# Performance work log

Measured on AMD Instinct MI355X. Metric: run time of the kernel, lower is better.

## Reference

```python
import jax, jax.numpy as jnp
import numpy as np

EPS = 1e-7
LAMBDA_RANK = 0.5
NEG = -1e30  # finite stand-in for -inf (keeps logsumexp grads finite)

B = 8192
N_BINS = 4


def setup_inputs() -> dict:
    key = jax.random.key(0)
    k1, k2, k3, k4 = jax.random.split(key, 4)
    outputs = jax.random.normal(k1, (B, N_BINS), dtype=jnp.float32)
    t = jax.random.uniform(k2, (B,), dtype=jnp.float32) * 100.0  # survival times
    y = jax.random.randint(k3, (B,), 0, N_BINS, dtype=jnp.int32)  # interval index
    c = jax.random.randint(k4, (B,), 0, 2, dtype=jnp.int32)       # 0=event, 1=censored
    return {"outputs": outputs, "t": t, "y": y, "c": c}


def reference(outputs, t, y, c):
    dt = outputs.dtype
    # ---- NLL survival loss ----
    hazards = jax.nn.sigmoid(outputs)                       # [B, K]
    S = jnp.cumprod(1.0 - hazards, axis=1)                  # [B, K]
    S_pad = jnp.concatenate([jnp.ones((outputs.shape[0], 1), dt), S], axis=1)  # [B, K+1]
    yv = y[:, None].astype(jnp.int32)
    s_prev = jnp.clip(jnp.take_along_axis(S_pad, yv, axis=1), EPS)
    h_this = jnp.clip(jnp.take_along_axis(hazards, yv, axis=1), EPS)
    s_this = jnp.clip(jnp.take_along_axis(S_pad, yv + 1, axis=1), EPS)
    cf = c[:, None].astype(dt)
    uncensored = -(1.0 - cf) * (jnp.log(s_prev) + jnp.log(h_this))
    censored = -cf * jnp.log(s_this)
    loss_nll = (censored + uncensored).mean()  # alpha == 0, reduction == 'mean'

    # ---- pairwise rank loss (vectorized over all i) ----
    risk = -jnp.sum(S, axis=1)                               # [B]
    event = (c == 0)                                         # [B] bool
    pair_mask = t[None, :] > t[:, None]                      # [B, B]; (i, j): t_j > t_i
    masked = jnp.where(pair_mask, risk[None, :], NEG)        # [B, B]
    lse = jax.nn.logsumexp(masked, axis=1)                   # [B]
    valid = event & jnp.any(pair_mask, axis=1)               # rows contributing
    contrib = jnp.where(valid, lse - risk, jnp.zeros((), dt))
    count = jnp.sum(valid.astype(dt))
    loss_rank = jnp.where(count > 0, contrib.sum() / jnp.maximum(count, 1.0), jnp.zeros((), dt))

    return loss_nll + LAMBDA_RANK * loss_rank
```

## Files before the change

kernel.cpp:

```cpp
#include <hip/hip_runtime.h>

#define BROWS 8192
#define EPSF 1e-7f
#define NBLK 256
#define RPB 32
#define TPB 1024

__device__ __forceinline__ float wave_reduce_sum(float v) {
    #pragma unroll
    for (int off = 32; off > 0; off >>= 1) v += __shfl_xor(v, off, 64);
    return v;
}
__device__ __forceinline__ float rcp_fast(float x) { return __builtin_amdgcn_rcpf(x); }

__device__ __forceinline__ float aload(const float* p) {
    return __hip_atomic_load(p, __ATOMIC_RELAXED, __HIP_MEMORY_SCOPE_AGENT);
}
__device__ __forceinline__ void astore(float* p, float v) {
    __hip_atomic_store(p, v, __ATOMIC_RELAXED, __HIP_MEMORY_SCOPE_AGENT);
}

__global__ __launch_bounds__(TPB, 4) void fused_kernel(
        const float4* __restrict__ outputs, const float* __restrict__ t,
        const int* __restrict__ y, const int* __restrict__ c,
        float* __restrict__ part, float* __restrict__ out) {
    __shared__ float2 te[BROWS];
    int tid = threadIdx.x, lane = tid & 63, wave = tid >> 6;
    int b = blockIdx.x;
    int rowbase = b * RPB;

    #pragma unroll
    for (int u = 0; u < BROWS / TPB; ++u) {
        int j = tid + u * TPB;
        float4 o = outputs[j];
        float q0 = rcp_fast(1.f + __expf(o.x));
        float q1 = rcp_fast(1.f + __expf(o.y));
        float q2 = rcp_fast(1.f + __expf(o.z));
        float q3 = rcp_fast(1.f + __expf(o.w));
        float S1 = q0, S2 = S1 * q1, S3 = S2 * q2, S4 = S3 * q3;
        float risk = -(S1 + S2 + S3 + S4);
        te[j] = make_float2(t[j], __expf(risk));
    }
    __syncthreads();

    float t0 = te[rowbase + 2 * wave].x;
    float t1 = te[rowbase + 2 * wave + 1].x;
    float a0 = 0.f, a1 = 0.f;
    const float4* te4 = (const float4*)te;
    #pragma unroll 8
    for (int k = lane; k < BROWS / 2; k += 64) {
        float4 q = te4[k];
        a0 += (q.x > t0) ? q.y : 0.f;
        a1 += (q.x > t1) ? q.y : 0.f;
        a0 += (q.z > t0) ? q.w : 0.f;
        a1 += (q.z > t1) ? q.w : 0.f;
    }
    a0 = wave_reduce_sum(a0);
    a1 = wave_reduce_sum(a1);
    __syncthreads();

    float* wsum = (float*)te;
    if (lane == 0) { wsum[2 * wave] = a0; wsum[2 * wave + 1] = a1; }
    __syncthreads();

    if (wave == 0) {
        float contrib = 0.f, cnt = 0.f, nll = 0.f;
        if (lane < RPB) {
            int row = rowbase + lane;
            float s = wsum[lane];
            float4 o = outputs[row];
            float q0 = rcp_fast(1.f + __expf(o.x));
            float q1 = rcp_fast(1.f + __expf(o.y));
            float q2 = rcp_fast(1.f + __expf(o.z));
            float q3 = rcp_fast(1.f + __expf(o.w));
            float S1 = q0, S2 = S1 * q1, S3 = S2 * q2, S4 = S3 * q3;
            float risk = -(S1 + S2 + S3 + S4);
            int yi = y[row], ci = c[row];
            float s_prev = (yi == 0) ? 1.f : (yi == 1) ? S1 : (yi == 2) ? S2 : S3;
            float s_this = (yi == 0) ? S1  : (yi == 1) ? S2 : (yi == 2) ? S3 : S4;
            float xsel   = (yi == 0) ? o.x : (yi == 1) ? o.y : (yi == 2) ? o.z : o.w;
            float h_this = rcp_fast(1.f + __expf(-xsel));
            float cf = (float)ci;
            nll = -cf * __logf(fmaxf(s_this, EPSF))
                  - (1.f - cf) * (__logf(fmaxf(s_prev, EPSF)) + __logf(fmaxf(h_this, EPSF)));
            bool valid = (ci == 0) && (s > 0.f);
            contrib = valid ? (__logf(s) - risk) : 0.f;
            cnt     = valid ? 1.f : 0.f;
        }
        contrib = wave_reduce_sum(contrib);
        cnt     = wave_reduce_sum(cnt);
        nll     = wave_reduce_sum(nll);
        if (lane == 0) {
            astore(&part[b * 4 + 0], contrib);
            astore(&part[b * 4 + 1], cnt);
            astore(&part[b * 4 + 2], nll);
            asm volatile("s_waitcnt vmcnt(0)" ::: "memory");
            astore(&part[b * 4 + 3], 1.0f);
        }
    }

    if (b == 0 && wave == 0) {
        int p0 = lane * 4;
        for (int sweep = 0; sweep < (1 << 17); ++sweep) {
            int ok = 1;
            #pragma unroll
            for (int k = 0; k < 4; ++k)
                ok &= (aload(&part[(p0 + k) * 4 + 3]) == 1.0f);
            if (__all(ok)) break;
            __builtin_amdgcn_s_sleep(8);
        }
        asm volatile("" ::: "memory");
        float rs = 0.f, cs = 0.f, ns = 0.f;
        #pragma unroll
        for (int k = 0; k < 4; ++k) {
            int pb = (p0 + k) * 4;
            rs += aload(&part[pb + 0]);
            cs += aload(&part[pb + 1]);
            ns += aload(&part[pb + 2]);
        }
        rs = wave_reduce_sum(rs);
        cs = wave_reduce_sum(cs);
        ns = wave_reduce_sum(ns);
        if (lane == 0) {
            float loss_nll  = ns / (float)BROWS;
            float loss_rank = (cs > 0.f) ? (rs / fmaxf(cs, 1.f)) : 0.f;
            out[0] = loss_nll + 0.5f * loss_rank;
        }
    }
}

extern "C" void kernel_launch(void* const* d_in, const int* in_sizes, int n_in,
                              void* d_out, int out_size, void* d_ws, size_t ws_size,
                              hipStream_t stream) {
    const float4* outputs = (const float4*)d_in[0];
    const float*  t       = (const float*)d_in[1];
    const int*    y       = (const int*)d_in[2];
    const int*    c       = (const int*)d_in[3];
    float* out  = (float*)d_out;
    float* part = (float*)d_ws;

    fused_kernel<<<NBLK, TPB, 0, stream>>>(outputs, t, y, c, part, out);
}
```

Measured before the change: 16.56 us.

## Replace O(B^2) pairwise sums with bucketed suffix-sum plus in-bucket correction

Each block now bins every exp(risk) into 4096 time buckets with shared-memory atomics and builds a suffix sum with a wave scan. Each row reads the suffix beyond its bucket and adds same-bucket entries through a staged list, replacing the full 8192-element scan per row. Block count halves to 128 with 64 rows each. The bucket scale 40.96 assumes t lies in [0,100), which matches the test inputs. Values outside that range are clamped into the edge buckets, still corrected by the in-bucket list, and rows are lost only if the stage capacity of 2048 overflows.

New measurement: 42.20 us. 155% more time.

```diff
diff --git a/kernel.cpp b/kernel.cpp
--- a/kernel.cpp
+++ b/kernel.cpp
@@ -1,36 +1,60 @@
 #include <hip/hip_runtime.h>
 
 #define BROWS 8192
-#define EPSF 1e-7f
-#define NBLK 256
-#define RPB 32
-#define TPB 1024
+#define NB    4096
+#define EPSF  1e-7f
+#define NBLK  128
+#define RPB   64
+#define TPB   1024
+#define IPT   (BROWS / TPB)
+#define SCAP  2048
 
 __device__ __forceinline__ float wave_reduce_sum(float v) {
     #pragma unroll
     for (int off = 32; off > 0; off >>= 1) v += __shfl_xor(v, off, 64);
     return v;
 }
+__device__ __forceinline__ float wave_incl_scan(float v, int lane) {
+    #pragma unroll
+    for (int off = 1; off < 64; off <<= 1) {
+        float u = __shfl_up(v, off, 64);
+        if (lane >= off) v += u;
+    }
+    return v;
+}
 __device__ __forceinline__ float rcp_fast(float x) { return __builtin_amdgcn_rcpf(x); }
-
 __device__ __forceinline__ float aload(const float* p) {
     return __hip_atomic_load(p, __ATOMIC_RELAXED, __HIP_MEMORY_SCOPE_AGENT);
 }
 __device__ __forceinline__ void astore(float* p, float v) {
     __hip_atomic_store(p, v, __ATOMIC_RELAXED, __HIP_MEMORY_SCOPE_AGENT);
 }
+__device__ __forceinline__ int bucket_of(float t) {
+    int b = (int)(t * 40.96f);
+    return min(max(b, 0), NB - 1);
+}
 
 __global__ __launch_bounds__(TPB, 4) void fused_kernel(
         const float4* __restrict__ outputs, const float* __restrict__ t,
         const int* __restrict__ y, const int* __restrict__ c,
         float* __restrict__ part, float* __restrict__ out) {
-    __shared__ float2 te[BROWS];
+    __shared__ float esum[NB];
+    __shared__ float suf[NB + 1];
+    __shared__ unsigned char rowhit[NB];
+    __shared__ float2 stage_te[SCAP];
+    __shared__ unsigned short stage_b[SCAP];
+    __shared__ int stage_n;
+    __shared__ float wtot[16];
+
     int tid = threadIdx.x, lane = tid & 63, wave = tid >> 6;
-    int b = blockIdx.x;
-    int rowbase = b * RPB;
+    int rowbase = blockIdx.x * RPB;
 
+    for (int k = tid; k < NB; k += TPB) { esum[k] = 0.f; rowhit[k] = 0; }
+    if (tid == 0) stage_n = 0;
+
+    float it_t[IPT], it_e[IPT]; int it_b[IPT];
     #pragma unroll
-    for (int u = 0; u < BROWS / TPB; ++u) {
+    for (int u = 0; u < IPT; ++u) {
         int j = tid + u * TPB;
         float4 o = outputs[j];
         float q0 = rcp_fast(1.f + __expf(o.x));
@@ -39,80 +63,102 @@
         float q3 = rcp_fast(1.f + __expf(o.w));
         float S1 = q0, S2 = S1 * q1, S3 = S2 * q2, S4 = S3 * q3;
         float risk = -(S1 + S2 + S3 + S4);
-        te[j] = make_float2(t[j], __expf(risk));
+        float tj = t[j];
+        it_t[u] = tj;
+        it_e[u] = __expf(risk);
+        it_b[u] = bucket_of(tj);
     }
     __syncthreads();
 
-    float t0 = te[rowbase + 2 * wave].x;
-    float t1 = te[rowbase + 2 * wave + 1].x;
-    float a0 = 0.f, a1 = 0.f;
-    const float4* te4 = (const float4*)te;
-    #pragma unroll 8
-    for (int k = lane; k < BROWS / 2; k += 64) {
-        float4 q = te4[k];
-        a0 += (q.x > t0) ? q.y : 0.f;
-        a1 += (q.x > t1) ? q.y : 0.f;
-        a0 += (q.z > t0) ? q.w : 0.f;
-        a1 += (q.z > t1) ? q.w : 0.f;
-    }
-    a0 = wave_reduce_sum(a0);
-    a1 = wave_reduce_sum(a1);
+    if (wave == 0) rowhit[bucket_of(t[rowbase + lane])] = 1;
+    #pragma unroll
+    for (int u = 0; u < IPT; ++u) atomicAdd(&esum[it_b[u]], it_e[u]);
     __syncthreads();
 
-    float* wsum = (float*)te;
-    if (lane == 0) { wsum[2 * wave] = a0; wsum[2 * wave + 1] = a1; }
+    {
+        int base = 4 * tid;
+        int i0 = NB - 1 - base;
+        float4 vv = *(const float4*)&esum[i0 - 3];
+        float v0 = vv.w, v1 = vv.z, v2 = vv.y, v3 = vv.x;
+        float s01 = v0 + v1, s012 = s01 + v2, s = s012 + v3;
+        float inc = wave_incl_scan(s, lane);
+        if (lane == 63) wtot[wave] = inc;
+        __syncthreads();
+        float wofs = 0.f;
+        #pragma unroll
+        for (int w = 0; w < 16; ++w) wofs += (w < wave) ? wtot[w] : 0.f;
+        float excl = wofs + inc - s;
+        float4 so;
+        so.x = excl + s; so.y = excl + s012; so.z = excl + s01; so.w = excl + v0;
+        *(float4*)&suf[i0 - 3] = so;
+        if (tid == 0) suf[NB] = 0.f;
+    }
+
+    #pragma unroll
+    for (int u = 0; u < IPT; ++u) {
+        if (rowhit[it_b[u]]) {
+            int p = atomicAdd(&stage_n, 1);
+            if (p < SCAP) {
+                stage_te[p] = make_float2(it_t[u], it_e[u]);
+                stage_b[p]  = (unsigned short)it_b[u];
+            }
+        }
+    }
     __syncthreads();
 
     if (wave == 0) {
-        float contrib = 0.f, cnt = 0.f, nll = 0.f;
-        if (lane < RPB) {
-            int row = rowbase + lane;
-            float s = wsum[lane];
-            float4 o = outputs[row];
-            float q0 = rcp_fast(1.f + __expf(o.x));
-            float q1 = rcp_fast(1.f + __expf(o.y));
-            float q2 = rcp_fast(1.f + __expf(o.z));
-            float q3 = rcp_fast(1.f + __expf(o.w));
-            float S1 = q0, S2 = S1 * q1, S3 = S2 * q2, S4 = S3 * q3;
-            float risk = -(S1 + S2 + S3 + S4);
-            int yi = y[row], ci = c[row];
-            float s_prev = (yi == 0) ? 1.f : (yi == 1) ? S1 : (yi == 2) ? S2 : S3;
-            float s_this = (yi == 0) ? S1  : (yi == 1) ? S2 : (yi == 2) ? S3 : S4;
-            float xsel   = (yi == 0) ? o.x : (yi == 1) ? o.y : (yi == 2) ? o.z : o.w;
-            float h_this = rcp_fast(1.f + __expf(-xsel));
-            float cf = (float)ci;
-            nll = -cf * __logf(fmaxf(s_this, EPSF))
-                  - (1.f - cf) * (__logf(fmaxf(s_prev, EPSF)) + __logf(fmaxf(h_this, EPSF)));
-            bool valid = (ci == 0) && (s > 0.f);
-            contrib = valid ? (__logf(s) - risk) : 0.f;
-            cnt     = valid ? 1.f : 0.f;
+        int row = rowbase + lane;
+        float tr = t[row];
+        int br = bucket_of(tr);
+        float s = suf[br + 1];
+        int n = min(stage_n, SCAP);
+        for (int k = 0; k < n; ++k) {
+            float2 p = stage_te[k];
+            s += (stage_b[k] == (unsigned short)br && p.x > tr) ? p.y : 0.f;
         }
+        float4 o = outputs[row];
+        float q0 = rcp_fast(1.f + __expf(o.x));
+        float q1 = rcp_fast(1.f + __expf(o.y));
+        float q2 = rcp_fast(1.f + __expf(o.z));
+        float q3 = rcp_fast(1.f + __expf(o.w));
+        float S1 = q0, S2 = S1 * q1, S3 = S2 * q2, S4 = S3 * q3;
+        float risk = -(S1 + S2 + S3 + S4);
+        int yi = y[row], ci = c[row];
+        float s_prev = (yi == 0) ? 1.f : (yi == 1) ? S1 : (yi == 2) ? S2 : S3;
+        float s_this = (yi == 0) ? S1  : (yi == 1) ? S2 : (yi == 2) ? S3 : S4;
+        float xsel   = (yi == 0) ? o.x : (yi == 1) ? o.y : (yi == 2) ? o.z : o.w;
+        float h_this = rcp_fast(1.f + __expf(-xsel));
+        float cf = (float)ci;
+        float nll = -cf * __logf(fmaxf(s_this, EPSF))
+                    - (1.f - cf) * (__logf(fmaxf(s_prev, EPSF)) + __logf(fmaxf(h_this, EPSF)));
+        bool valid = (ci == 0) && (s > 0.f);
+        float contrib = valid ? (__logf(s) - risk) : 0.f;
+        float cnt     = valid ? 1.f : 0.f;
         contrib = wave_reduce_sum(contrib);
         cnt     = wave_reduce_sum(cnt);
         nll     = wave_reduce_sum(nll);
         if (lane == 0) {
-            astore(&part[b * 4 + 0], contrib);
-            astore(&part[b * 4 + 1], cnt);
-            astore(&part[b * 4 + 2], nll);
+            int pb = blockIdx.x * 4;
+            astore(&part[pb + 0], contrib);
+            astore(&part[pb + 1], cnt);
+            astore(&part[pb + 2], nll);
             asm volatile("s_waitcnt vmcnt(0)" ::: "memory");
-            astore(&part[b * 4 + 3], 1.0f);
+            astore(&part[pb + 3], 1.0f);
         }
     }
 
-    if (b == 0 && wave == 0) {
-        int p0 = lane * 4;
+    if (blockIdx.x == 0 && wave == 1) {
+        int p0 = lane * 2;
         for (int sweep = 0; sweep < (1 << 17); ++sweep) {
-            int ok = 1;
-            #pragma unroll
-            for (int k = 0; k < 4; ++k)
-                ok &= (aload(&part[(p0 + k) * 4 + 3]) == 1.0f);
+            int ok = (aload(&part[p0 * 4 + 3]) == 1.0f) &
+                     (aload(&part[(p0 + 1) * 4 + 3]) == 1.0f);
             if (__all(ok)) break;
             __builtin_amdgcn_s_sleep(8);
         }
         asm volatile("" ::: "memory");
         float rs = 0.f, cs = 0.f, ns = 0.f;
         #pragma unroll
-        for (int k = 0; k < 4; ++k) {
+        for (int k = 0; k < 2; ++k) {
             int pb = (p0 + k) * 4;
             rs += aload(&part[pb + 0]);
             cs += aload(&part[pb + 1]);
```

## Process four rows per wave over half the columns to raise LDS reuse

Applied to the files above, without the earlier changes.

Each wave now compares four target rows against half of the shared-memory column array instead of two rows against the full array, with wave pairs splitting the columns. Each LDS float4 load now feeds twice as many comparisons, which halves total LDS traffic in the pairwise pass. The partial sums go into a dedicated shared array, which removes one __syncthreads. The cost is more accumulator registers, one extra cross-half add, and a smaller unroll factor.

Result: faster. 15.90 us (-3.9%).

```diff
diff --git a/kernel.cpp b/kernel.cpp
--- a/kernel.cpp
+++ b/kernel.cpp
@@ -25,6 +25,8 @@
         const int* __restrict__ y, const int* __restrict__ c,
         float* __restrict__ part, float* __restrict__ out) {
     __shared__ float2 te[BROWS];
+    __shared__ float wsum[2][RPB];
+
     int tid = threadIdx.x, lane = tid & 63, wave = tid >> 6;
     int b = blockIdx.x;
     int rowbase = b * RPB;
@@ -43,31 +45,45 @@
     }
     __syncthreads();
 
-    float t0 = te[rowbase + 2 * wave].x;
-    float t1 = te[rowbase + 2 * wave + 1].x;
-    float a0 = 0.f, a1 = 0.f;
+    int p = wave >> 1, half = wave & 1;
+    int r0 = rowbase + 4 * p;
+    float t0 = te[r0 + 0].x;
+    float t1 = te[r0 + 1].x;
+    float t2 = te[r0 + 2].x;
+    float t3 = te[r0 + 3].x;
+
+    float a0 = 0.f, a1 = 0.f, a2 = 0.f, a3 = 0.f;
     const float4* te4 = (const float4*)te;
-    #pragma unroll 8
-    for (int k = lane; k < BROWS / 2; k += 64) {
+    int kbeg = half * 2048 + lane;
+    #pragma unroll 4
+    for (int k = kbeg; k < kbeg - lane + 2048; k += 64) {
         float4 q = te4[k];
         a0 += (q.x > t0) ? q.y : 0.f;
         a1 += (q.x > t1) ? q.y : 0.f;
+        a2 += (q.x > t2) ? q.y : 0.f;
+        a3 += (q.x > t3) ? q.y : 0.f;
         a0 += (q.z > t0) ? q.w : 0.f;
         a1 += (q.z > t1) ? q.w : 0.f;
+        a2 += (q.z > t2) ? q.w : 0.f;
+        a3 += (q.z > t3) ? q.w : 0.f;
     }
     a0 = wave_reduce_sum(a0);
     a1 = wave_reduce_sum(a1);
-    __syncthreads();
-
-    float* wsum = (float*)te;
-    if (lane == 0) { wsum[2 * wave] = a0; wsum[2 * wave + 1] = a1; }
+    a2 = wave_reduce_sum(a2);
+    a3 = wave_reduce_sum(a3);
+    if (lane == 0) {
+        wsum[half][4 * p + 0] = a0;
+        wsum[half][4 * p + 1] = a1;
+        wsum[half][4 * p + 2] = a2;
+        wsum[half][4 * p + 3] = a3;
+    }
     __syncthreads();
 
     if (wave == 0) {
         float contrib = 0.f, cnt = 0.f, nll = 0.f;
         if (lane < RPB) {
             int row = rowbase + lane;
-            float s = wsum[lane];
+            float s = wsum[0][lane] + wsum[1][lane];
             float4 o = outputs[row];
             float q0 = rcp_fast(1.f + __expf(o.x));
             float q1 = rcp_fast(1.f + __expf(o.y));
```
